# Optimization experiments

Measured on AMD Instinct MI355X. Metric: run time of the kernel, lower is better.

Reference implementation:

```python
import jax, jax.numpy as jnp
import numpy as np

B, N, D, H, HD, HID, RP_HID = 4, 512, 1024, 16, 64, 4096, 64
EPS = 1e-5


def _ln(h, g, b):
    mu = h.mean(-1, keepdims=True)
    var = h.var(-1, keepdims=True)
    return (h - mu) / jnp.sqrt(var + EPS) * g + b


def setup_inputs() -> dict:
    key = jax.random.key(0)
    ks = jax.random.split(key, 24)
    s = 0.05
    return {
        "x": jax.random.normal(ks[0], (B, N, D), jnp.float32),
        "t_emb": jax.random.normal(ks[1], (B, D), jnp.float32),
        "rel_pos_matrix": jax.random.normal(ks[2], (B, N, N, 2), jnp.float32),
        "agent_mask": jax.random.randint(ks[3], (B, N), 0, 2).astype(jnp.int32),
        # adaLN modulation: Linear(D, 6D)
        "w_ada": jax.random.normal(ks[4], (6 * D, D), jnp.float32) * s,
        "b_ada": jnp.zeros((6 * D,), jnp.float32),
        # LayerNorms
        "g1": jnp.ones((D,), jnp.float32),
        "beta1": jnp.zeros((D,), jnp.float32),
        "g2": jnp.ones((D,), jnp.float32),
        "beta2": jnp.zeros((D,), jnp.float32),
        # attention qkv / proj
        "w_qkv": jax.random.normal(ks[5], (3 * D, D), jnp.float32) * s,
        "b_qkv": jnp.zeros((3 * D,), jnp.float32),
        "w_proj": jax.random.normal(ks[6], (D, D), jnp.float32) * s,
        "b_proj": jnp.zeros((D,), jnp.float32),
        # rel-pos bias MLP: Linear(2,64) -> ReLU -> Linear(64,H)
        "w_rp1": jax.random.normal(ks[7], (RP_HID, 2), jnp.float32) * s,
        "b_rp1": jnp.zeros((RP_HID,), jnp.float32),
        "w_rp2": jax.random.normal(ks[8], (H, RP_HID), jnp.float32) * s,
        "b_rp2": jnp.zeros((H,), jnp.float32),
        # MLP: Linear(D, HID) -> GELU -> Linear(HID, D)
        "w_fc1": jax.random.normal(ks[9], (HID, D), jnp.float32) * s,
        "b_fc1": jnp.zeros((HID,), jnp.float32),
        "w_fc2": jax.random.normal(ks[10], (D, HID), jnp.float32) * s,
        "b_fc2": jnp.zeros((D,), jnp.float32),
    }


def reference(x, t_emb, rel_pos_matrix, agent_mask,
              w_ada, b_ada, g1, beta1, w_qkv, b_qkv, w_proj, b_proj,
              w_rp1, b_rp1, w_rp2, b_rp2, g2, beta2,
              w_fc1, b_fc1, w_fc2, b_fc2):
    b, n, d = x.shape
    # adaLN: SiLU -> Linear -> 6 chunks of [B, D]
    mod = jax.nn.silu(t_emb) @ w_ada.T + b_ada
    shift_s, scale_s, gate_s, shift_m, scale_m, gate_m = jnp.split(mod, 6, axis=1)

    # ---- spatial attention branch ----
    xn = _ln(x, g1, beta1) * (1.0 + scale_s[:, None, :]) + shift_s[:, None, :]
    qkv = (xn @ w_qkv.T + b_qkv).reshape(b, n, 3, H, HD)
    q, k, v = jnp.moveaxis(qkv, 2, 0)  # each [B, N, H, HD]
    attn = jnp.einsum('bnhd,bmhd->bhnm', q, k) * (HD ** -0.5)
    # relative-position bias MLP: [B,N,N,2] -> [B,N,N,H] -> [B,H,N,N]
    bias = jax.nn.relu(rel_pos_matrix @ w_rp1.T + b_rp1) @ w_rp2.T + b_rp2
    attn = attn + bias.transpose(0, 3, 1, 2)
    mask = agent_mask.astype(bool)[:, None, None, :]  # key-side mask [B,1,1,N]
    attn = jnp.where(mask, attn, -jnp.inf)
    p = jax.nn.softmax(attn, axis=-1)
    out = jnp.einsum('bhnm,bmhd->bnhd', p, v).reshape(b, n, d)
    out = out @ w_proj.T + b_proj
    x = x + gate_s[:, None, :] * out

    # ---- gated MLP branch ----
    xn = _ln(x, g2, beta2) * (1.0 + scale_m[:, None, :]) + shift_m[:, None, :]
    h = jax.nn.gelu(xn @ w_fc1.T + b_fc1, approximate=False)
    x = x + gate_m[:, None, :] * (h @ w_fc2.T + b_fc2)
    return x
```

## Files before the change

kernel.cpp:

```cpp
#include <hip/hip_runtime.h>


#define B_ 4
#define N_ 512
#define D_ 1024
#define H_ 16
#define HID_ 4096
#define M_ (B_*N_)

typedef unsigned short u16;
typedef __attribute__((ext_vector_type(8))) short bf16x8;
typedef __attribute__((ext_vector_type(4))) float f32x4;

__device__ __forceinline__ float b2f(u16 u){
  union { unsigned int i; float f; } x; x.i = ((unsigned int)u) << 16; return x.f;
}
__device__ __forceinline__ u16 f2b(float f){
  unsigned int u = __float_as_uint(f);
  return (u16)((u + 0x7fffu + ((u >> 16) & 1u)) >> 16);
}

__device__ __forceinline__ void gload16(const u16* __restrict__ g, u16* l){
#if defined(__has_builtin) && __has_builtin(__builtin_amdgcn_global_load_lds)
  __builtin_amdgcn_global_load_lds(
      (const __attribute__((address_space(1))) unsigned int*)g,
      (__attribute__((address_space(3))) unsigned int*)l, 16, 0, 0);
#else
  *(uint4*)l = *(const uint4*)g;
#endif
}

__global__ __launch_bounds__(256) void k_cvt(const float* __restrict__ s, u16* __restrict__ d){
  size_t i = ((size_t)blockIdx.x*256 + threadIdx.x)*8;
  float4 a = *(const float4*)(s+i), b = *(const float4*)(s+i+4);
  u16 o[8] = {f2b(a.x),f2b(a.y),f2b(a.z),f2b(a.w),f2b(b.x),f2b(b.y),f2b(b.z),f2b(b.w)};
  *(uint4*)(d+i) = *(const uint4*)o;
}

__global__ __launch_bounds__(256) void k_mod(const float* __restrict__ t_emb,
    const float* __restrict__ w_ada, const float* __restrict__ b_ada,
    float* __restrict__ mod)
{
  __shared__ float st[D_];
  int b = blockIdx.y;
  for (int i = threadIdx.x; i < D_; i += 256){
    float x = t_emb[b*D_ + i];
    st[i] = x / (1.f + __expf(-x));
  }
  __syncthreads();
  int j = blockIdx.x * 256 + threadIdx.x;
  const float* wr = w_ada + (size_t)j * D_;
  float acc = b_ada[j];
  for (int k = 0; k < D_; k += 8){
    float4 p0 = *(const float4*)(wr + k);
    float4 p1 = *(const float4*)(wr + k + 4);
    acc += p0.x*st[k+0] + p0.y*st[k+1] + p0.z*st[k+2] + p0.w*st[k+3];
    acc += p1.x*st[k+4] + p1.y*st[k+5] + p1.z*st[k+6] + p1.w*st[k+7];
  }
  mod[b*6*D_ + j] = acc;
}

__global__ __launch_bounds__(256) void k_lnmod(const float* __restrict__ xin,
    const float* __restrict__ g, const float* __restrict__ be,
    const float* __restrict__ mod, int shift_idx, int scale_idx,
    u16* __restrict__ xn)
{
  int row = blockIdx.x;
  int b = row >> 9;
  float v[4]; float s = 0.f, s2 = 0.f;
  #pragma unroll
  for (int i=0;i<4;i++){
    float x = xin[(size_t)row*D_ + threadIdx.x + i*256];
    v[i] = x; s += x; s2 += x*x;
  }
  #pragma unroll
  for (int o=32;o>0;o>>=1){ s += __shfl_down(s,o); s2 += __shfl_down(s2,o); }
  __shared__ float rs[4], rs2[4];
  int w = threadIdx.x >> 6;
  if ((threadIdx.x & 63)==0){ rs[w]=s; rs2[w]=s2; }
  __syncthreads();
  s = rs[0]+rs[1]+rs[2]+rs[3]; s2 = rs2[0]+rs2[1]+rs2[2]+rs2[3];
  float mu = s * (1.f/D_);
  float var = s2 * (1.f/D_) - mu*mu;
  float rstd = rsqrtf(var + 1e-5f);
  const float* mrow = mod + b*6*D_;
  #pragma unroll
  for (int i=0;i<4;i++){
    int d = threadIdx.x + i*256;
    float xg = (v[i]-mu)*rstd*g[d] + be[d];
    xn[(size_t)row*D_ + d] = f2b(xg * (1.f + mrow[scale_idx*D_ + d]) + mrow[shift_idx*D_ + d]);
  }
}

__global__ __launch_bounds__(256) void k_bias(const float* __restrict__ rel,
    const int* __restrict__ amask,
    const float* __restrict__ w_rp1, const float* __restrict__ b_rp1,
    const float* __restrict__ w_rp2, const float* __restrict__ b_rp2,
    u16* __restrict__ biasbuf)
{
  __shared__ __align__(16) u16 Hs[256*72];
  __shared__ __align__(16) u16 Bs[16*272];
  __shared__ __align__(16) u16 w2s[16*72];
  __shared__ float b2s[16];
  __shared__ u16 msk[256];
  int mh = blockIdx.x, n = blockIdx.y, b = blockIdx.z;
  int tid = threadIdx.x;
  int w = tid >> 6, lane = tid & 63, ln = lane & 15, quad = lane >> 4;

  for (int i = tid; i < 1024; i += 256) w2s[(i>>6)*72 + (i&63)] = f2b(w_rp2[i]);
  if (tid < 16) b2s[tid] = b_rp2[tid];
  msk[tid] = (u16)(amask[b*N_ + mh*256 + tid] != 0);

  {
    float2 r01 = *(const float2*)(rel + ((size_t)((b*N_ + n)*N_) + mh*256 + tid)*2);
    const float* w1 = w_rp1;
    u16 hv[64];
    #pragma unroll
    for (int j=0;j<64;j++){
      float t = w1[2*j]*r01.x + w1[2*j+1]*r01.y + b_rp1[j];
      hv[j] = f2b(t > 0.f ? t : 0.f);
    }
    uint4* dst = (uint4*)&Hs[tid*72];
    #pragma unroll
    for (int c=0;c<8;c++) dst[c] = *(const uint4*)&hv[c*8];
  }
  __syncthreads();

  bf16x8 af0 = *(const bf16x8*)&w2s[ln*72 + quad*8];
  bf16x8 af1 = *(const bf16x8*)&w2s[ln*72 + 32 + quad*8];

  #pragma unroll
  for (int t=0; t<4; t++){
    int mt = w*4 + t;
    bf16x8 bf0 = *(const bf16x8*)&Hs[(mt*16+ln)*72 + quad*8];
    bf16x8 bf1 = *(const bf16x8*)&Hs[(mt*16+ln)*72 + 32 + quad*8];
    f32x4 c = {};
    c = __builtin_amdgcn_mfma_f32_16x16x32_bf16(af0, bf0, c, 0,0,0);
    c = __builtin_amdgcn_mfma_f32_16x16x32_bf16(af1, bf1, c, 0,0,0);
    bool valid = msk[mt*16 + ln] != 0;
    #pragma unroll
    for (int i=0;i<4;i++){
      int h = quad*4 + i;
      float val = valid ? (c[i] + b2s[h]) : -1e30f;
      Bs[h*272 + mt*16 + ln] = f2b(val);
    }
  }
  __syncthreads();

  #pragma unroll
  for (int it=0; it<8; it++){
    int idx = it*256 + tid;
    int r = idx >> 7, cc = idx & 127;
    size_t rb = (((size_t)(b*H_ + r)*N_) + n)*N_ + mh*256;
    ((unsigned int*)(biasbuf + rb))[cc] = ((const unsigned int*)(Bs + r*272))[cc];
  }
}

enum { EPI_QKV=0, EPI_FC1=1, EPI_PART=2 };

template<int EPI>
__global__ __launch_bounds__(256) void k_gemm(const u16* __restrict__ A,
    const u16* __restrict__ W, const float* __restrict__ Wb, int K, int Kslice,
    float* __restrict__ o_f32, u16* __restrict__ o_u16)
{
  __shared__ __align__(16) u16 Al[128*64];
  __shared__ __align__(16) u16 Wl[128*64];
  int row0 = blockIdx.y*128, col0 = blockIdx.x*128;
  int tid = threadIdx.x;
  int w = tid >> 6, lane = tid & 63, ln = lane & 15, quad = lane >> 4;
  int wy = w >> 1, wx = w & 1;
  int srow = tid >> 3;
  int schunk = (tid & 7) ^ (srow & 7);
  const u16* Ag = A + (size_t)(row0 + srow)*K + schunk*8;
  const u16* Wg = W + (size_t)(col0 + srow)*K + schunk*8;
  int aoff[4][2], woff[4][2];
  #pragma unroll
  for (int ms=0; ms<4; ms++){
    int r = 64*wy + 16*ms + ln;
    #pragma unroll
    for (int kk=0; kk<2; kk++)
      aoff[ms][kk] = r*64 + (((kk*4+quad) ^ (ln&7))*8);
  }
  #pragma unroll
  for (int ns=0; ns<4; ns++){
    int r = 64*wx + 16*ns + ln;
    #pragma unroll
    for (int kk=0; kk<2; kk++)
      woff[ns][kk] = r*64 + (((kk*4+quad) ^ (ln&7))*8);
  }
  f32x4 acc[4][4] = {};
  int kbeg = blockIdx.z * Kslice;
  for (int k0 = kbeg; k0 < kbeg + Kslice; k0 += 64){
    #pragma unroll
    for (int i=0;i<4;i++){
      gload16(Ag + k0 + (size_t)(32*i)*K, Al + i*2048 + tid*8);
      gload16(Wg + k0 + (size_t)(32*i)*K, Wl + i*2048 + tid*8);
    }
    __syncthreads();
    #pragma unroll
    for (int kk=0; kk<2; kk++){
      bf16x8 af[4], bfr[4];
      #pragma unroll
      for (int ms=0; ms<4; ms++) af[ms]  = *(const bf16x8*)&Al[aoff[ms][kk]];
      #pragma unroll
      for (int ns=0; ns<4; ns++) bfr[ns] = *(const bf16x8*)&Wl[woff[ns][kk]];
      #pragma unroll
      for (int ms=0; ms<4; ms++)
        #pragma unroll
        for (int ns=0; ns<4; ns++)
          acc[ms][ns] = __builtin_amdgcn_mfma_f32_16x16x32_bf16(af[ms], bfr[ns], acc[ms][ns], 0,0,0);
    }
    __syncthreads();
  }

  #pragma unroll
  for (int ms=0; ms<4; ms++){
    #pragma unroll
    for (int ns=0; ns<4; ns++){
      int c = col0 + 64*wx + 16*ns + ln;
      float wb = (EPI == EPI_PART) ? 0.f : Wb[c];
      #pragma unroll
      for (int i=0;i<4;i++){
        int r = row0 + 64*wy + 16*ms + quad*4 + i;
        float val = acc[ms][ns][i] + wb;
        if (EPI == EPI_QKV){
          o_u16[(size_t)r*3072 + c] = f2b(val);
        } else if (EPI == EPI_FC1){
          float gl = 0.5f*val*(1.f + erff(val*0.70710678f));
          o_u16[(size_t)r*HID_ + c] = f2b(gl);
        } else {
          o_u16[((size_t)blockIdx.z*M_ + r)*D_ + c] = f2b(val);
        }
      }
    }
  }
}

template<int GIDX>
__global__ __launch_bounds__(256) void k_red(const u16* __restrict__ part,
    const float* __restrict__ Wb, const float* __restrict__ mod,
    const float* __restrict__ resid, float* __restrict__ outp)
{
  size_t i = ((size_t)blockIdx.x*256 + threadIdx.x)*4;
  int c = (int)(i & 1023); int r = (int)(i >> 10); int b = r >> 9;
  uint2 p0 = *(const uint2*)(part + i);
  uint2 p1 = *(const uint2*)(part + (size_t)M_*D_ + i);
  float4 pv;
  pv.x = b2f((u16)(p0.x & 0xffff)) + b2f((u16)(p1.x & 0xffff));
  pv.y = b2f((u16)(p0.x >> 16))    + b2f((u16)(p1.x >> 16));
  pv.z = b2f((u16)(p0.y & 0xffff)) + b2f((u16)(p1.y & 0xffff));
  pv.w = b2f((u16)(p0.y >> 16))    + b2f((u16)(p1.y >> 16));
  float4 x4 = *(const float4*)(resid + i);
  float4 bi = *(const float4*)(Wb + c);
  float4 g4 = *(const float4*)(mod + b*6*D_ + GIDX*D_ + c);
  float4 o;
  o.x = x4.x + g4.x*(pv.x + bi.x);
  o.y = x4.y + g4.y*(pv.y + bi.y);
  o.z = x4.z + g4.z*(pv.z + bi.z);
  o.w = x4.w + g4.w*(pv.w + bi.w);
  *(float4*)(outp + i) = o;
}

__global__ __launch_bounds__(512) void k_attn(const u16* __restrict__ qkv,
    const u16* __restrict__ biasbuf, u16* __restrict__ attn_out)
{
  __shared__ __align__(16) u16 Qs[128*72];
  __shared__ __align__(16) u16 Ks[64*72];
  __shared__ __align__(16) u16 Vt[64*72];
  __shared__ __align__(16) u16 Ps[8*16*72];
  int nt = blockIdx.x, h = blockIdx.y, b = blockIdx.z;
  int n0 = nt*128;
  int tid = threadIdx.x;
  int w = tid >> 6, lane = tid & 63, ln = lane & 15, quad = lane >> 4;

  {
    int row = tid >> 2, cb = (tid & 3)*16;
    const u16* src = qkv + (size_t)(b*N_ + n0 + row)*3072 + h*64 + cb;
    uint4 q0 = *(const uint4*)src, q1 = *(const uint4*)(src+8);
    uint4* dst = (uint4*)&Qs[row*72 + cb];
    dst[0] = q0; dst[1] = q1;
  }
  __syncthreads();
  bf16x8 qf[2];
  qf[0] = *(const bf16x8*)&Qs[(16*w+ln)*72 + quad*8];
  qf[1] = *(const bf16x8*)&Qs[(16*w+ln)*72 + 32 + quad*8];

  f32x4 oacc[4] = {};
  float rmax[4] = {-3e38f,-3e38f,-3e38f,-3e38f};
  float rsum[4] = {0.f,0.f,0.f,0.f};
  const u16* bp = biasbuf + (((size_t)(b*H_ + h)*N_) + n0 + 16*w)*N_ + ln;

  for (int mt = 0; mt < 8; mt++){
    __syncthreads();
    {
      int r = tid >> 3, cb = (tid & 7)*8;
      const u16* kp = qkv + (size_t)(b*N_ + mt*64 + r)*3072 + 1024 + h*64 + cb;
      *(uint4*)&Ks[r*72 + cb] = *(const uint4*)kp;
      const u16* vp = qkv + (size_t)(b*N_ + mt*64 + r)*3072 + 2048 + h*64 + cb;
      uint4 vv = *(const uint4*)vp;
      u16 ve[8] = { (u16)(vv.x&0xffff),(u16)(vv.x>>16),(u16)(vv.y&0xffff),(u16)(vv.y>>16),
                    (u16)(vv.z&0xffff),(u16)(vv.z>>16),(u16)(vv.w&0xffff),(u16)(vv.w>>16) };
      #pragma unroll
      for (int j=0;j<8;j++) Vt[(cb+j)*72 + r] = ve[j];
    }
    __syncthreads();

    u16 bl[4][4];
    #pragma unroll
    for (int cs=0; cs<4; cs++)
      #pragma unroll
      for (int i=0;i<4;i++)
        bl[cs][i] = bp[(size_t)(quad*4+i)*N_ + mt*64 + 16*cs];

    f32x4 s[4];
    #pragma unroll
    for (int cs=0; cs<4; cs++){
      bf16x8 k0f = *(const bf16x8*)&Ks[(16*cs+ln)*72 + quad*8];
      bf16x8 k1f = *(const bf16x8*)&Ks[(16*cs+ln)*72 + 32 + quad*8];
      f32x4 z = {};
      z = __builtin_amdgcn_mfma_f32_16x16x32_bf16(qf[0], k0f, z, 0,0,0);
      z = __builtin_amdgcn_mfma_f32_16x16x32_bf16(qf[1], k1f, z, 0,0,0);
      s[cs] = z;
    }
    #pragma unroll
    for (int cs=0; cs<4; cs++)
      #pragma unroll
      for (int i=0;i<4;i++)
        s[cs][i] = s[cs][i]*0.125f + b2f(bl[cs][i]);

    #pragma unroll
    for (int i=0;i<4;i++){
      float tm = fmaxf(fmaxf(s[0][i], s[1][i]), fmaxf(s[2][i], s[3][i]));
      #pragma unroll
      for (int o=1;o<16;o<<=1) tm = fmaxf(tm, __shfl_xor(tm, o));
      float nm = fmaxf(rmax[i], tm);
      float alpha = __expf(rmax[i] - nm);
      rmax[i] = nm;
      float ps = 0.f;
      #pragma unroll
      for (int cs=0; cs<4; cs++){
        float p = __expf(s[cs][i] - nm);
        s[cs][i] = p; ps += p;
      }
      #pragma unroll
      for (int o=1;o<16;o<<=1) ps += __shfl_xor(ps, o);
      rsum[i] = rsum[i]*alpha + ps;
      #pragma unroll
      for (int ds=0; ds<4; ds++) oacc[ds][i] *= alpha;
    }

    #pragma unroll
    for (int cs=0; cs<4; cs++)
      #pragma unroll
      for (int i=0;i<4;i++)
        Ps[w*1152 + (quad*4+i)*72 + 16*cs + ln] = f2b(s[cs][i]);

    bf16x8 pf0 = *(const bf16x8*)&Ps[w*1152 + ln*72 + quad*8];
    bf16x8 pf1 = *(const bf16x8*)&Ps[w*1152 + ln*72 + 32 + quad*8];
    #pragma unroll
    for (int ds=0; ds<4; ds++){
      bf16x8 v0f = *(const bf16x8*)&Vt[(16*ds+ln)*72 + quad*8];
      bf16x8 v1f = *(const bf16x8*)&Vt[(16*ds+ln)*72 + 32 + quad*8];
      oacc[ds] = __builtin_amdgcn_mfma_f32_16x16x32_bf16(pf0, v0f, oacc[ds], 0,0,0);
      oacc[ds] = __builtin_amdgcn_mfma_f32_16x16x32_bf16(pf1, v1f, oacc[ds], 0,0,0);
    }
  }

  #pragma unroll
  for (int i=0;i<4;i++){
    float inv = 1.f / rsum[i];
    int r = b*N_ + n0 + 16*w + quad*4 + i;
    #pragma unroll
    for (int ds=0; ds<4; ds++)
      attn_out[(size_t)r*D_ + h*64 + 16*ds + ln] = f2b(oacc[ds][i]*inv);
  }
}

extern "C" void kernel_launch(void* const* d_in, const int* in_sizes, int n_in,
                              void* d_out, int out_size, void* d_ws, size_t ws_size,
                              hipStream_t stream) {
  const float* x      = (const float*)d_in[0];
  const float* t_emb  = (const float*)d_in[1];
  const float* rel    = (const float*)d_in[2];
  const int*   amask  = (const int*)d_in[3];
  const float* w_ada  = (const float*)d_in[4];
  const float* b_ada  = (const float*)d_in[5];
  const float* g1     = (const float*)d_in[6];
  const float* beta1  = (const float*)d_in[7];
  const float* g2     = (const float*)d_in[8];
  const float* beta2  = (const float*)d_in[9];
  const float* w_qkv  = (const float*)d_in[10];
  const float* b_qkv  = (const float*)d_in[11];
  const float* w_proj = (const float*)d_in[12];
  const float* b_proj = (const float*)d_in[13];
  const float* w_rp1  = (const float*)d_in[14];
  const float* b_rp1  = (const float*)d_in[15];
  const float* w_rp2  = (const float*)d_in[16];
  const float* b_rp2  = (const float*)d_in[17];
  const float* w_fc1  = (const float*)d_in[18];
  const float* b_fc1  = (const float*)d_in[19];
  const float* w_fc2  = (const float*)d_in[20];
  const float* b_fc2  = (const float*)d_in[21];
  float* outp = (float*)d_out;

  const size_t MB = 1u<<20;
  char* wsb = (char*)d_ws;
  float* mod   = (float*)(wsb);
  u16*  xn     = (u16*) (wsb + 131072);
  float* xm    = (float*)(wsb + 131072 + 4*MB);
  u16*  wqkvb  = (u16*) (wsb + 131072 + 12*MB);
  u16*  wprojb = (u16*) (wsb + 131072 + 18*MB);
  u16*  partb  = (u16*) (wsb + 131072 + 20*MB);
  char*  S     = wsb + 131072 + 28*MB;
  u16*  qkvb   = (u16*)(S);
  u16*  biasb  = (u16*)(S + 12*MB);
  u16*  hb     = (u16*)(S);
  u16*  wfc1b  = (u16*)(S + 16*MB);
  u16*  wfc2b  = (u16*)(S + 24*MB);

  k_cvt<<<1536, 256, 0, stream>>>(w_qkv,  wqkvb);
  k_cvt<<<512,  256, 0, stream>>>(w_proj, wprojb);
  k_mod<<<dim3(6*D_/256, B_), 256, 0, stream>>>(t_emb, w_ada, b_ada, mod);
  k_bias<<<dim3(2, N_, B_), 256, 0, stream>>>(rel, amask, w_rp1, b_rp1, w_rp2, b_rp2, biasb);
  k_lnmod<<<M_, 256, 0, stream>>>(x, g1, beta1, mod, 0, 1, xn);
  k_gemm<EPI_QKV><<<dim3(3072/128, M_/128), 256, 0, stream>>>(
      xn, wqkvb, b_qkv, D_, D_, nullptr, qkvb);
  k_attn<<<dim3(4, H_, B_), 512, 0, stream>>>(qkvb, biasb, xn);
  k_cvt<<<2048, 256, 0, stream>>>(w_fc1, wfc1b);
  k_cvt<<<2048, 256, 0, stream>>>(w_fc2, wfc2b);
  k_gemm<EPI_PART><<<dim3(D_/128, M_/128, 2), 256, 0, stream>>>(
      xn, wprojb, nullptr, D_, D_/2, nullptr, partb);
  k_red<2><<<2048, 256, 0, stream>>>(partb, b_proj, mod, x, xm);
  k_lnmod<<<M_, 256, 0, stream>>>(xm, g2, beta2, mod, 3, 4, xn);
  k_gemm<EPI_FC1><<<dim3(HID_/128, M_/128), 256, 0, stream>>>(
      xn, wfc1b, b_fc1, D_, D_, nullptr, hb);
  k_gemm<EPI_PART><<<dim3(D_/128, M_/128, 2), 256, 0, stream>>>(
      hb, wfc2b, nullptr, HID_, HID_/2, nullptr, partb);
  k_red<5><<<2048, 256, 0, stream>>>(partb, b_fc2, mod, xm, outp);
}
```

Baseline: 373.9 us.

## Split-K QKV, proj and FC2 GEMMs more finely and shrink attention blocks

The QKV GEMM becomes a 2-way split-K with a separate bf16 reduction kernel, and the proj and FC2 GEMMs move from 2-way to 4-way split-K with a 4-input reduction. The attention kernel drops from 128-query to 64-query blocks with 256 threads, doubling the grid, and the weight conversion launches are merged in pairs. The goal is more blocks on the many CUs and fewer launches. The cost is extra partial-sum traffic through memory, more bf16 rounding of partials, and more K/V reloads per query row in attention.

```diff
diff --git a/kernel.cpp b/kernel.cpp
--- a/kernel.cpp
+++ b/kernel.cpp
@@ -30,8 +30,12 @@
 #endif
 }
 
-__global__ __launch_bounds__(256) void k_cvt(const float* __restrict__ s, u16* __restrict__ d){
-  size_t i = ((size_t)blockIdx.x*256 + threadIdx.x)*8;
+__global__ __launch_bounds__(256) void k_cvt2(const float* __restrict__ sA, u16* __restrict__ dA,
+    int nA, const float* __restrict__ sB, u16* __restrict__ dB){
+  int blk = blockIdx.x;
+  const float* s; u16* d; size_t i;
+  if (blk < nA){ s = sA; d = dA; i = ((size_t)blk*256 + threadIdx.x)*8; }
+  else { s = sB; d = dB; i = ((size_t)(blk-nA)*256 + threadIdx.x)*8; }
   float4 a = *(const float4*)(s+i), b = *(const float4*)(s+i+4);
   u16 o[8] = {f2b(a.x),f2b(a.y),f2b(a.z),f2b(a.w),f2b(b.x),f2b(b.y),f2b(b.z),f2b(b.w)};
   *(uint4*)(d+i) = *(const uint4*)o;
@@ -156,12 +160,12 @@
   }
 }
 
-enum { EPI_QKV=0, EPI_FC1=1, EPI_PART=2 };
+enum { EPI_FC1=0, EPI_PART=1 };
 
 template<int EPI>
 __global__ __launch_bounds__(256) void k_gemm(const u16* __restrict__ A,
     const u16* __restrict__ W, const float* __restrict__ Wb, int K, int Kslice,
-    float* __restrict__ o_f32, u16* __restrict__ o_u16)
+    int ldc, u16* __restrict__ part01, u16* __restrict__ part23)
 {
   __shared__ __align__(16) u16 Al[128*64];
   __shared__ __align__(16) u16 Wl[128*64];
@@ -213,43 +217,63 @@
     __syncthreads();
   }
 
+  u16* pbase = (EPI == EPI_PART)
+             ? ((blockIdx.z < 2 ? part01 : part23) + (size_t)(blockIdx.z & 1)*M_*ldc)
+             : part01;
   #pragma unroll
   for (int ms=0; ms<4; ms++){
     #pragma unroll
     for (int ns=0; ns<4; ns++){
       int c = col0 + 64*wx + 16*ns + ln;
-      float wb = (EPI == EPI_PART) ? 0.f : Wb[c];
+      float wb = (EPI == EPI_FC1) ? Wb[c] : 0.f;
       #pragma unroll
       for (int i=0;i<4;i++){
         int r = row0 + 64*wy + 16*ms + quad*4 + i;
         float val = acc[ms][ns][i] + wb;
-        if (EPI == EPI_QKV){
-          o_u16[(size_t)r*3072 + c] = f2b(val);
-        } else if (EPI == EPI_FC1){
+        if (EPI == EPI_FC1){
           float gl = 0.5f*val*(1.f + erff(val*0.70710678f));
-          o_u16[(size_t)r*HID_ + c] = f2b(gl);
+          pbase[(size_t)r*ldc + c] = f2b(gl);
         } else {
-          o_u16[((size_t)blockIdx.z*M_ + r)*D_ + c] = f2b(val);
+          pbase[(size_t)r*ldc + c] = f2b(val);
         }
       }
     }
   }
 }
 
+__global__ __launch_bounds__(256) void k_redq(const u16* __restrict__ part,
+    const float* __restrict__ Wb, u16* __restrict__ qkvb)
+{
+  size_t i = ((size_t)blockIdx.x*256 + threadIdx.x)*4;
+  int c = (int)(i % 3072);
+  uint2 p0 = *(const uint2*)(part + i);
+  uint2 p1 = *(const uint2*)(part + (size_t)M_*3072 + i);
+  float4 bi = *(const float4*)(Wb + c);
+  u16 o[4];
+  o[0] = f2b(b2f((u16)(p0.x & 0xffff)) + b2f((u16)(p1.x & 0xffff)) + bi.x);
+  o[1] = f2b(b2f((u16)(p0.x >> 16))    + b2f((u16)(p1.x >> 16))    + bi.y);
+  o[2] = f2b(b2f((u16)(p0.y & 0xffff)) + b2f((u16)(p1.y & 0xffff)) + bi.z);
+  o[3] = f2b(b2f((u16)(p0.y >> 16))    + b2f((u16)(p1.y >> 16))    + bi.w);
+  *(uint2*)(qkvb + i) = *(const uint2*)o;
+}
+
 template<int GIDX>
-__global__ __launch_bounds__(256) void k_red(const u16* __restrict__ part,
-    const float* __restrict__ Wb, const float* __restrict__ mod,
-    const float* __restrict__ resid, float* __restrict__ outp)
+__global__ __launch_bounds__(256) void k_red4(const u16* __restrict__ p01,
+    const u16* __restrict__ p23, const float* __restrict__ Wb,
+    const float* __restrict__ mod, const float* __restrict__ resid,
+    float* __restrict__ outp)
 {
   size_t i = ((size_t)blockIdx.x*256 + threadIdx.x)*4;
   int c = (int)(i & 1023); int r = (int)(i >> 10); int b = r >> 9;
-  uint2 p0 = *(const uint2*)(part + i);
-  uint2 p1 = *(const uint2*)(part + (size_t)M_*D_ + i);
+  uint2 a0 = *(const uint2*)(p01 + i);
+  uint2 a1 = *(const uint2*)(p01 + (size_t)M_*D_ + i);
+  uint2 a2 = *(const uint2*)(p23 + i);
+  uint2 a3 = *(const uint2*)(p23 + (size_t)M_*D_ + i);
   float4 pv;
-  pv.x = b2f((u16)(p0.x & 0xffff)) + b2f((u16)(p1.x & 0xffff));
-  pv.y = b2f((u16)(p0.x >> 16))    + b2f((u16)(p1.x >> 16));
-  pv.z = b2f((u16)(p0.y & 0xffff)) + b2f((u16)(p1.y & 0xffff));
-  pv.w = b2f((u16)(p0.y >> 16))    + b2f((u16)(p1.y >> 16));
+  pv.x = b2f((u16)(a0.x&0xffff)) + b2f((u16)(a1.x&0xffff)) + b2f((u16)(a2.x&0xffff)) + b2f((u16)(a3.x&0xffff));
+  pv.y = b2f((u16)(a0.x>>16))    + b2f((u16)(a1.x>>16))    + b2f((u16)(a2.x>>16))    + b2f((u16)(a3.x>>16));
+  pv.z = b2f((u16)(a0.y&0xffff)) + b2f((u16)(a1.y&0xffff)) + b2f((u16)(a2.y&0xffff)) + b2f((u16)(a3.y&0xffff));
+  pv.w = b2f((u16)(a0.y>>16))    + b2f((u16)(a1.y>>16))    + b2f((u16)(a2.y>>16))    + b2f((u16)(a3.y>>16));
   float4 x4 = *(const float4*)(resid + i);
   float4 bi = *(const float4*)(Wb + c);
   float4 g4 = *(const float4*)(mod + b*6*D_ + GIDX*D_ + c);
@@ -261,15 +285,15 @@
   *(float4*)(outp + i) = o;
 }
 
-__global__ __launch_bounds__(512) void k_attn(const u16* __restrict__ qkv,
+__global__ __launch_bounds__(256) void k_attn(const u16* __restrict__ qkv,
     const u16* __restrict__ biasbuf, u16* __restrict__ attn_out)
 {
-  __shared__ __align__(16) u16 Qs[128*72];
+  __shared__ __align__(16) u16 Qs[64*72];
   __shared__ __align__(16) u16 Ks[64*72];
   __shared__ __align__(16) u16 Vt[64*72];
-  __shared__ __align__(16) u16 Ps[8*16*72];
+  __shared__ __align__(16) u16 Ps[4*16*72];
   int nt = blockIdx.x, h = blockIdx.y, b = blockIdx.z;
-  int n0 = nt*128;
+  int n0 = nt*64;
   int tid = threadIdx.x;
   int w = tid >> 6, lane = tid & 63, ln = lane & 15, quad = lane >> 4;
 
@@ -293,15 +317,17 @@
   for (int mt = 0; mt < 8; mt++){
     __syncthreads();
     {
-      int r = tid >> 3, cb = (tid & 7)*8;
+      int r = tid >> 2, cb = (tid & 3)*16;
       const u16* kp = qkv + (size_t)(b*N_ + mt*64 + r)*3072 + 1024 + h*64 + cb;
-      *(uint4*)&Ks[r*72 + cb] = *(const uint4*)kp;
+      uint4 k0 = *(const uint4*)kp, k1 = *(const uint4*)(kp+8);
+      uint4* kd = (uint4*)&Ks[r*72 + cb];
+      kd[0] = k0; kd[1] = k1;
       const u16* vp = qkv + (size_t)(b*N_ + mt*64 + r)*3072 + 2048 + h*64 + cb;
-      uint4 vv = *(const uint4*)vp;
-      u16 ve[8] = { (u16)(vv.x&0xffff),(u16)(vv.x>>16),(u16)(vv.y&0xffff),(u16)(vv.y>>16),
-                    (u16)(vv.z&0xffff),(u16)(vv.z>>16),(u16)(vv.w&0xffff),(u16)(vv.w>>16) };
-      #pragma unroll
-      for (int j=0;j<8;j++) Vt[(cb+j)*72 + r] = ve[j];
+      uint4 v0 = *(const uint4*)vp, v1 = *(const uint4*)(vp+8);
+      u16 ve[16];
+      *(uint4*)&ve[0] = v0; *(uint4*)&ve[8] = v1;
+      #pragma unroll
+      for (int j=0;j<16;j++) Vt[(cb+j)*72 + r] = ve[j];
     }
     __syncthreads();
 
@@ -413,28 +439,30 @@
   u16*  partb  = (u16*) (wsb + 131072 + 20*MB);
   char*  S     = wsb + 131072 + 28*MB;
   u16*  qkvb   = (u16*)(S);
+  u16*  qkvpart= (u16*)(S + 12*MB);
   u16*  biasb  = (u16*)(S + 12*MB);
+  u16*  projp23= (u16*)(S);
   u16*  hb     = (u16*)(S);
   u16*  wfc1b  = (u16*)(S + 16*MB);
   u16*  wfc2b  = (u16*)(S + 24*MB);
-
-  k_cvt<<<1536, 256, 0, stream>>>(w_qkv,  wqkvb);
-  k_cvt<<<512,  256, 0, stream>>>(w_proj, wprojb);
+  u16*  fc2p23 = (u16*)(S + 32*MB);
+
+  k_cvt2<<<2048, 256, 0, stream>>>(w_qkv, wqkvb, 1536, w_proj, wprojb);
   k_mod<<<dim3(6*D_/256, B_), 256, 0, stream>>>(t_emb, w_ada, b_ada, mod);
+  k_lnmod<<<M_, 256, 0, stream>>>(x, g1, beta1, mod, 0, 1, xn);
+  k_gemm<EPI_PART><<<dim3(3072/128, M_/128, 2), 256, 0, stream>>>(
+      xn, wqkvb, nullptr, D_, D_/2, 3072, qkvpart, qkvpart);
+  k_redq<<<6144, 256, 0, stream>>>(qkvpart, b_qkv, qkvb);
   k_bias<<<dim3(2, N_, B_), 256, 0, stream>>>(rel, amask, w_rp1, b_rp1, w_rp2, b_rp2, biasb);
-  k_lnmod<<<M_, 256, 0, stream>>>(x, g1, beta1, mod, 0, 1, xn);
-  k_gemm<EPI_QKV><<<dim3(3072/128, M_/128), 256, 0, stream>>>(
-      xn, wqkvb, b_qkv, D_, D_, nullptr, qkvb);
-  k_attn<<<dim3(4, H_, B_), 512, 0, stream>>>(qkvb, biasb, xn);
-  k_cvt<<<2048, 256, 0, stream>>>(w_fc1, wfc1b);
-  k_cvt<<<2048, 256, 0, stream>>>(w_fc2, wfc2b);
-  k_gemm<EPI_PART><<<dim3(D_/128, M_/128, 2), 256, 0, stream>>>(
-      xn, wprojb, nullptr, D_, D_/2, nullptr, partb);
-  k_red<2><<<2048, 256, 0, stream>>>(partb, b_proj, mod, x, xm);
+  k_attn<<<dim3(8, H_, B_), 256, 0, stream>>>(qkvb, biasb, xn);
+  k_cvt2<<<4096, 256, 0, stream>>>(w_fc1, wfc1b, 2048, w_fc2, wfc2b);
+  k_gemm<EPI_PART><<<dim3(D_/128, M_/128, 4), 256, 0, stream>>>(
+      xn, wprojb, nullptr, D_, D_/4, D_, partb, projp23);
+  k_red4<2><<<2048, 256, 0, stream>>>(partb, projp23, b_proj, mod, x, xm);
   k_lnmod<<<M_, 256, 0, stream>>>(xm, g2, beta2, mod, 3, 4, xn);
   k_gemm<EPI_FC1><<<dim3(HID_/128, M_/128), 256, 0, stream>>>(
-      xn, wfc1b, b_fc1, D_, D_, nullptr, hb);
-  k_gemm<EPI_PART><<<dim3(D_/128, M_/128, 2), 256, 0, stream>>>(
-      hb, wfc2b, nullptr, HID_, HID_/2, nullptr, partb);
-  k_red<5><<<2048, 256, 0, stream>>>(partb, b_fc2, mod, xm, outp);
-}
+      xn, wfc1b, b_fc1, D_, D_, HID_, hb, nullptr);
+  k_gemm<EPI_PART><<<dim3(D_/128, M_/128, 4), 256, 0, stream>>>(
+      hb, wfc2b, nullptr, HID_, HID_/4, D_, partb, fc2p23);
+  k_red4<5><<<2048, 256, 0, stream>>>(partb, fc2p23, b_fc2, mod, xm, outp);
+}
```

Measured after the change: 369.5 us. No clear change (-1.2%).
